# Performance work log

Hardware: AMD Instinct MI355X
Metric: run time of the kernel (lower is better)

Reference implementation:

```python
import jax, jax.numpy as jnp
import numpy as np

OUT = 260        # RESIZE_OUTPUT_IMAGES_SHAPE
TH = 0.8         # OD_SCORE_TH
PCT = 1.0        # INTERNAL_PERCENTAGE_IMAGE_TOTAKE
N_BOXES = 10     # loop bound in original call()
TAPS = 6         # lanczos3 support (radius 3 -> 6 taps, antialias=False)


def _lanczos_taps(src, size):
    """src: (OUT,) float sample coords in crop-local space; size: traced int crop size.
    Returns clamped tap indices (OUT,6) and normalized lanczos3 weights (OUT,6)."""
    base = jnp.floor(src).astype(jnp.int32) - 2
    taps = base[:, None] + jnp.arange(TAPS, dtype=jnp.int32)          # (OUT,6)
    d = src[:, None] - taps.astype(src.dtype)
    w = jnp.where(jnp.abs(d) < 3.0, jnp.sinc(d) * jnp.sinc(d / 3.0), 0.0)
    w = w / jnp.sum(w, axis=1, keepdims=True)
    idx = jnp.clip(taps, 0, size - 1)
    return idx, w


def _crop_resize(img, box):
    """img: (H,W,3). box: (4,) normalized [ymin,xmin,ymax,xmax] -> (OUT,OUT,3).
    Matches tf.image.resize lanczos3 (antialias=False): half-pixel centers, clamped edges."""
    H, W = img.shape[0], img.shape[1]
    y0 = (box[0] * H).astype(jnp.int32)
    x0 = (box[1] * W).astype(jnp.int32)
    y1 = (box[2] * H).astype(jnp.int32)
    x1 = (box[3] * W).astype(jnp.int32)
    ch = jnp.maximum(y1 - y0, 1)
    cw = jnp.maximum(x1 - x0, 1)
    o = jnp.arange(OUT, dtype=img.dtype)
    src_h = (o + 0.5) * (ch.astype(img.dtype) / OUT) - 0.5
    src_w = (o + 0.5) * (cw.astype(img.dtype) / OUT) - 0.5
    idx_h, w_h = _lanczos_taps(src_h, ch)
    idx_w, w_w = _lanczos_taps(src_w, cw)
    idx_h = idx_h + y0
    idx_w = idx_w + x0
    # vertical pass: gather 6 row taps per output row, reduce -> (OUT, W, 3)
    rows = jnp.einsum('pa,pawc->pwc', w_h, img[idx_h])
    # horizontal pass: gather 6 col taps per output col, reduce -> (OUT, OUT, 3)
    out = jnp.einsum('qb,pqbc->pqc', w_w, rows[:, idx_w])
    return out


def setup_inputs() -> dict:
    key = jax.random.key(0)
    k1, k2, k3, k4 = jax.random.split(key, 4)
    # scores: first 10 mostly above threshold, rest below
    s_hi = 0.85 + 0.15 * jax.random.uniform(k1, (N_BOXES,), dtype=jnp.float32)
    s_lo = 0.8 * jax.random.uniform(k2, (100 - N_BOXES,), dtype=jnp.float32)
    od_scores = jnp.concatenate([s_hi, s_lo])
    # bboxes (ymin,xmin,ymax,xmax) with guaranteed positive crop sizes
    u = jax.random.uniform(k3, (100, 4), dtype=jnp.float32)
    od_bboxes = jnp.stack([u[:, 0] * 0.45, u[:, 1] * 0.45,
                           0.55 + 0.45 * u[:, 2], 0.55 + 0.45 * u[:, 3]], axis=1)
    image = jax.random.normal(k4, (1, 2048, 2048, 3), dtype=jnp.float32)
    return {"od_scores": od_scores, "od_bboxes": od_bboxes, "image": image}


def reference(od_scores, od_bboxes, image):
    img = image[0]                           # (H,W,3)
    b10 = od_bboxes[:N_BOXES]
    s10 = od_scores[:N_BOXES]
    valid = ((od_scores[0] >= TH) & (s10 >= TH)
             & (b10[:, 1] >= 0.5 - PCT / 2.0)
             & (b10[:, 3] <= 0.5 + PCT / 2.0))
    crops = jax.vmap(lambda b: _crop_resize(img, b))(b10)   # (10,OUT,OUT,3)
    return crops * valid[:, None, None, None].astype(img.dtype)
```

## Files before the change

### kernel.cpp

```cpp
#include <hip/hip_runtime.h>
#include <math.h>

#define OUT 260
#define TAPS 6
#define IMG_H 2048
#define IMG_W 2048
#define ROW_F (IMG_W * 3)
#define NB 10
#define TH 0.8f
#define QB 65
#define SEGS 4
#define LDSF 1600

__device__ __forceinline__ float sincf(float x) {
    if (x == 0.0f) return 1.0f;
    float px = 3.14159265358979323846f * x;
    return __sinf(px) / px;
}


__global__ __launch_bounds__(320) void tables_kernel(
    const float* __restrict__ scores, const float* __restrict__ boxes,
    float* __restrict__ htab, float* __restrict__ vtab)
{
    const int box = blockIdx.x;
    const float b0 = boxes[box * 4 + 0];
    const float b1 = boxes[box * 4 + 1];
    const float b2 = boxes[box * 4 + 2];
    const float b3 = boxes[box * 4 + 3];

    const int y0 = (int)(b0 * (float)IMG_H);
    const int x0 = (int)(b1 * (float)IMG_W);
    const int y1 = (int)(b2 * (float)IMG_H);
    const int x1 = (int)(b3 * (float)IMG_W);
    const int ch = max(y1 - y0, 1);
    const int cw = max(x1 - x0, 1);

    const bool valid = (scores[0] >= TH) && (scores[box] >= TH)
                    && (b1 >= 0.0f) && (b3 <= 1.0f);
    const float vmask = valid ? 1.0f : 0.0f;

    const int t = threadIdx.x;
    if (t >= OUT) return;

    {
        const float src = ((float)t + 0.5f) * ((float)cw / (float)OUT) - 0.5f;
        const int base = (int)floorf(src) - 2;
        float w[TAPS]; int id[TAPS];
        float s = 0.0f;
        #pragma unroll
        for (int k = 0; k < TAPS; ++k) {
            const float d = src - (float)(base + k);
            const float wv = (fabsf(d) < 3.0f) ? sincf(d) * sincf(d * (1.0f / 3.0f)) : 0.0f;
            w[k] = wv; s += wv;
            int tt = base + k; tt = tt < 0 ? 0 : tt; tt = tt > cw - 1 ? cw - 1 : tt;
            id[k] = (x0 + tt) * 3;
        }
        const float inv = 1.0f / s;
        float* h = htab + ((size_t)(box * OUT + t) << 4);
        int*   hi = (int*)h;
        #pragma unroll
        for (int k = 0; k < TAPS; ++k) { h[k] = w[k] * inv; hi[8 + k] = id[k]; }
        h[6] = 0.0f; h[7] = 0.0f; hi[14] = 0; hi[15] = 0;
    }

    {
        const float src = ((float)t + 0.5f) * ((float)ch / (float)OUT) - 0.5f;
        const int base = (int)floorf(src) - 2;
        float w[TAPS]; int id[TAPS];
        float s = 0.0f;
        #pragma unroll
        for (int k = 0; k < TAPS; ++k) {
            const float d = src - (float)(base + k);
            const float wv = (fabsf(d) < 3.0f) ? sincf(d) * sincf(d * (1.0f / 3.0f)) : 0.0f;
            w[k] = wv; s += wv;
            int tt = base + k; tt = tt < 0 ? 0 : tt; tt = tt > ch - 1 ? ch - 1 : tt;
            id[k] = tt + y0;
        }
        const float inv = vmask / s;
        float* v = vtab + ((size_t)(box * OUT + t) << 4);
        int*   vi = (int*)v;
        #pragma unroll
        for (int k = 0; k < TAPS; ++k) { v[k] = w[k] * inv; vi[8 + k] = id[k]; }
        v[6] = 0.0f; v[7] = 0.0f; vi[14] = 0; vi[15] = 0;
    }
}

__global__ __launch_bounds__(64) void crop_resize_seg(
    const float* __restrict__ img,
    const float* __restrict__ htab,
    const float* __restrict__ vtab,
    float* __restrict__ out)
{
    const int seg = blockIdx.x;
    const int p   = blockIdx.y;
    const int box = blockIdx.z;
    const int q0  = seg * QB;

    const float* vrec = vtab + ((size_t)(box * OUT + p) << 4);
    const int*   vi   = (const int*)vrec;
    float wh[TAPS]; int rows[TAPS];
    #pragma unroll
    for (int k = 0; k < TAPS; ++k) { wh[k] = vrec[k]; rows[k] = vi[8 + k]; }

    const int* hi_first = (const int*)(htab + ((size_t)(box * OUT + q0) << 4));
    const int* hi_last  = (const int*)(htab + ((size_t)(box * OUT + q0 + QB - 1) << 4));
    const int start_f = hi_first[8] & ~3;
    const int n_f     = ((hi_last[13] + 3) - start_f + 3) & ~3;

    __shared__ float lds[LDSF];

    {
        const float* r0 = img + (size_t)rows[0] * ROW_F + start_f;
        const float* r1 = img + (size_t)rows[1] * ROW_F + start_f;
        const float* r2 = img + (size_t)rows[2] * ROW_F + start_f;
        const float* r3 = img + (size_t)rows[3] * ROW_F + start_f;
        const float* r4 = img + (size_t)rows[4] * ROW_F + start_f;
        const float* r5 = img + (size_t)rows[5] * ROW_F + start_f;

        for (int f = threadIdx.x * 4; f < n_f; f += 64 * 4) {
            const float4 v0 = *(const float4*)(r0 + f);
            const float4 v1 = *(const float4*)(r1 + f);
            const float4 v2 = *(const float4*)(r2 + f);
            const float4 v3 = *(const float4*)(r3 + f);
            const float4 v4 = *(const float4*)(r4 + f);
            const float4 v5 = *(const float4*)(r5 + f);
            float4 acc;
            acc.x = wh[0]*v0.x + wh[1]*v1.x + wh[2]*v2.x + wh[3]*v3.x + wh[4]*v4.x + wh[5]*v5.x;
            acc.y = wh[0]*v0.y + wh[1]*v1.y + wh[2]*v2.y + wh[3]*v3.y + wh[4]*v4.y + wh[5]*v5.y;
            acc.z = wh[0]*v0.z + wh[1]*v1.z + wh[2]*v2.z + wh[3]*v3.z + wh[4]*v4.z + wh[5]*v5.z;
            acc.w = wh[0]*v0.w + wh[1]*v1.w + wh[2]*v2.w + wh[3]*v3.w + wh[4]*v4.w + wh[5]*v5.w;
            *(float4*)(lds + f) = acc;
        }
    }
    __syncthreads();

    for (int qi = threadIdx.x; qi < QB; qi += 64) {
        const int q = q0 + qi;
        const float* h  = htab + ((size_t)(box * OUT + q) << 4);
        const int*   hi = (const int*)h;
        float a0 = 0.0f, a1 = 0.0f, a2 = 0.0f;
        #pragma unroll
        for (int k = 0; k < TAPS; ++k) {
            const float w  = h[k];
            const int   li = hi[8 + k] - start_f;
            a0 = fmaf(w, lds[li + 0], a0);
            a1 = fmaf(w, lds[li + 1], a1);
            a2 = fmaf(w, lds[li + 2], a2);
        }
        const size_t o = (((size_t)box * OUT + p) * OUT + q) * 3;
        out[o + 0] = a0;
        out[o + 1] = a1;
        out[o + 2] = a2;
    }
}

__global__ __launch_bounds__(256) void crop_resize_fallback(
    const float* __restrict__ scores, const float* __restrict__ boxes,
    const float* __restrict__ img, float* __restrict__ out)
{
    const int p = blockIdx.x, box = blockIdx.y;
    const float b0 = boxes[box*4+0], b1 = boxes[box*4+1];
    const float b2 = boxes[box*4+2], b3 = boxes[box*4+3];
    const int y0 = (int)(b0*(float)IMG_H), x0 = (int)(b1*(float)IMG_W);
    const int y1 = (int)(b2*(float)IMG_H), x1 = (int)(b3*(float)IMG_W);
    const int ch = max(y1-y0,1), cw = max(x1-x0,1);
    const bool valid = (scores[0]>=TH)&&(scores[box]>=TH)&&(b1>=0.0f)&&(b3<=1.0f);
    const float vmask = valid?1.0f:0.0f;
    float wh[TAPS]; int ih[TAPS];
    {
        const float src = ((float)p+0.5f)*((float)ch/(float)OUT)-0.5f;
        const int base = (int)floorf(src)-2;
        float s = 0.0f;
        #pragma unroll
        for (int a = 0; a < TAPS; ++a) {
            const float d = src-(float)(base+a);
            const float w = (fabsf(d)<3.0f)?sincf(d)*sincf(d*(1.0f/3.0f)):0.0f;
            wh[a]=w; s+=w;
            int t=base+a; t=t<0?0:t; t=t>ch-1?ch-1:t; ih[a]=t+y0;
        }
        const float inv = 1.0f/s;
        #pragma unroll
        for (int a = 0; a < TAPS; ++a) wh[a]*=inv;
    }
    const int start_f = (x0*3)&~3;
    const int end_f = (x0+cw)*3;
    const int n_f = end_f-start_f;
    __shared__ float lds[6152];
    {
        const float* r0 = img+(size_t)ih[0]*ROW_F+start_f;
        const float* r1 = img+(size_t)ih[1]*ROW_F+start_f;
        const float* r2 = img+(size_t)ih[2]*ROW_F+start_f;
        const float* r3 = img+(size_t)ih[3]*ROW_F+start_f;
        const float* r4 = img+(size_t)ih[4]*ROW_F+start_f;
        const float* r5 = img+(size_t)ih[5]*ROW_F+start_f;
        for (int f = threadIdx.x*4; f < n_f; f += 256*4) {
            const float4 v0=*(const float4*)(r0+f), v1=*(const float4*)(r1+f);
            const float4 v2=*(const float4*)(r2+f), v3=*(const float4*)(r3+f);
            const float4 v4=*(const float4*)(r4+f), v5=*(const float4*)(r5+f);
            float4 acc;
            acc.x=wh[0]*v0.x+wh[1]*v1.x+wh[2]*v2.x+wh[3]*v3.x+wh[4]*v4.x+wh[5]*v5.x;
            acc.y=wh[0]*v0.y+wh[1]*v1.y+wh[2]*v2.y+wh[3]*v3.y+wh[4]*v4.y+wh[5]*v5.y;
            acc.z=wh[0]*v0.z+wh[1]*v1.z+wh[2]*v2.z+wh[3]*v3.z+wh[4]*v4.z+wh[5]*v5.z;
            acc.w=wh[0]*v0.w+wh[1]*v1.w+wh[2]*v2.w+wh[3]*v3.w+wh[4]*v4.w+wh[5]*v5.w;
            *(float4*)(lds+f)=acc;
        }
    }
    __syncthreads();
    const float wscale = (float)cw/(float)OUT;
    for (int q = threadIdx.x; q < OUT; q += 256) {
        const float src = ((float)q+0.5f)*wscale-0.5f;
        const int basew = (int)floorf(src)-2;
        float ww[TAPS]; float s = 0.0f;
        #pragma unroll
        for (int k = 0; k < TAPS; ++k) {
            const float d = src-(float)(basew+k);
            const float w = (fabsf(d)<3.0f)?sincf(d)*sincf(d*(1.0f/3.0f)):0.0f;
            ww[k]=w; s+=w;
        }
        const float inv = 1.0f/s;
        float a0=0,a1=0,a2=0;
        #pragma unroll
        for (int k = 0; k < TAPS; ++k) {
            int t=basew+k; t=t<0?0:t; t=t>cw-1?cw-1:t;
            const int hb=(x0+t)*3-start_f;
            a0=fmaf(ww[k],lds[hb+0],a0);
            a1=fmaf(ww[k],lds[hb+1],a1);
            a2=fmaf(ww[k],lds[hb+2],a2);
        }
        const float m = vmask*inv;
        const size_t o = (((size_t)box*OUT+p)*OUT+q)*3;
        out[o+0]=a0*m; out[o+1]=a1*m; out[o+2]=a2*m;
    }
}

extern "C" void kernel_launch(void* const* d_in, const int* in_sizes, int n_in,
                              void* d_out, int out_size, void* d_ws, size_t ws_size,
                              hipStream_t stream) {
    const float* scores = (const float*)d_in[0];
    const float* boxes  = (const float*)d_in[1];
    const float* img    = (const float*)d_in[2];
    float* out = (float*)d_out;

    const size_t tab_bytes = (size_t)NB * OUT * 16 * sizeof(float);
    if (ws_size < 2 * tab_bytes) {
        crop_resize_fallback<<<dim3(OUT, NB), dim3(256), 0, stream>>>(scores, boxes, img, out);
        return;
    }
    float* htab = (float*)d_ws;
    float* vtab = (float*)((char*)d_ws + tab_bytes);

    tables_kernel<<<dim3(NB), dim3(320), 0, stream>>>(scores, boxes, htab, vtab);
    crop_resize_seg<<<dim3(SEGS, OUT, NB), dim3(64), 0, stream>>>(img, htab, vtab, out);
}
```

Before: 113.8 us.

## Fuse table precompute into single crop-resize kernel with XCD-aware block remap

```diff
diff --git a/kernel.cpp b/kernel.cpp
--- a/kernel.cpp
+++ b/kernel.cpp
@@ -8,9 +8,10 @@
 #define ROW_F (IMG_W * 3)
 #define NB 10
 #define TH 0.8f
-#define QB 65
-#define SEGS 4
-#define LDSF 1600
+#define LDSF 6152
+#define NXCD 8
+#define NWG (NB * OUT)
+#define CPX (NWG / NXCD)
 
 __device__ __forceinline__ float sincf(float x) {
     if (x == 0.0f) return 1.0f;
@@ -18,107 +19,77 @@
     return __sinf(px) / px;
 }
 
+__global__ __launch_bounds__(256) void crop_resize_one(
+    const float* __restrict__ scores, const float* __restrict__ boxes,
+    const float* __restrict__ img, float* __restrict__ out)
+{
+    const int bid  = blockIdx.x;
+    const int lbid = (bid & (NXCD - 1)) * CPX + (bid >> 3);
+    const int p    = lbid % OUT;
+    const int box  = lbid / OUT;
 
-__global__ __launch_bounds__(320) void tables_kernel(
-    const float* __restrict__ scores, const float* __restrict__ boxes,
-    float* __restrict__ htab, float* __restrict__ vtab)
-{
-    const int box = blockIdx.x;
     const float b0 = boxes[box * 4 + 0];
     const float b1 = boxes[box * 4 + 1];
     const float b2 = boxes[box * 4 + 2];
     const float b3 = boxes[box * 4 + 3];
-
     const int y0 = (int)(b0 * (float)IMG_H);
     const int x0 = (int)(b1 * (float)IMG_W);
     const int y1 = (int)(b2 * (float)IMG_H);
     const int x1 = (int)(b3 * (float)IMG_W);
     const int ch = max(y1 - y0, 1);
     const int cw = max(x1 - x0, 1);
-
     const bool valid = (scores[0] >= TH) && (scores[box] >= TH)
                     && (b1 >= 0.0f) && (b3 <= 1.0f);
     const float vmask = valid ? 1.0f : 0.0f;
 
-    const int t = threadIdx.x;
-    if (t >= OUT) return;
-
+    float wh[TAPS]; int ih[TAPS];
     {
-        const float src = ((float)t + 0.5f) * ((float)cw / (float)OUT) - 0.5f;
+        const float src = ((float)p + 0.5f) * ((float)ch / (float)OUT) - 0.5f;
         const int base = (int)floorf(src) - 2;
-        float w[TAPS]; int id[TAPS];
         float s = 0.0f;
         #pragma unroll
         for (int k = 0; k < TAPS; ++k) {
             const float d = src - (float)(base + k);
-            const float wv = (fabsf(d) < 3.0f) ? sincf(d) * sincf(d * (1.0f / 3.0f)) : 0.0f;
-            w[k] = wv; s += wv;
-            int tt = base + k; tt = tt < 0 ? 0 : tt; tt = tt > cw - 1 ? cw - 1 : tt;
-            id[k] = (x0 + tt) * 3;
+            const float w = (fabsf(d) < 3.0f) ? sincf(d) * sincf(d * (1.0f / 3.0f)) : 0.0f;
+            wh[k] = w; s += w;
+            int t = base + k; t = t < 0 ? 0 : t; t = t > ch - 1 ? ch - 1 : t;
+            ih[k] = t + y0;
         }
         const float inv = 1.0f / s;
-        float* h = htab + ((size_t)(box * OUT + t) << 4);
-        int*   hi = (int*)h;
         #pragma unroll
-        for (int k = 0; k < TAPS; ++k) { h[k] = w[k] * inv; hi[8 + k] = id[k]; }
-        h[6] = 0.0f; h[7] = 0.0f; hi[14] = 0; hi[15] = 0;
+        for (int k = 0; k < TAPS; ++k) wh[k] *= inv;
     }
 
+    const int start_f = (x0 * 3) & ~3;
+    const int n_f     = (x0 + cw) * 3 - start_f;
+
+    const int q = threadIdx.x;
+    const float wscale = (float)cw / (float)OUT;
+    float ww[TAPS]; int lb[TAPS]; float hm;
     {
-        const float src = ((float)t + 0.5f) * ((float)ch / (float)OUT) - 0.5f;
+        const float src = ((float)q + 0.5f) * wscale - 0.5f;
         const int base = (int)floorf(src) - 2;
-        float w[TAPS]; int id[TAPS];
         float s = 0.0f;
         #pragma unroll
         for (int k = 0; k < TAPS; ++k) {
             const float d = src - (float)(base + k);
-            const float wv = (fabsf(d) < 3.0f) ? sincf(d) * sincf(d * (1.0f / 3.0f)) : 0.0f;
-            w[k] = wv; s += wv;
-            int tt = base + k; tt = tt < 0 ? 0 : tt; tt = tt > ch - 1 ? ch - 1 : tt;
-            id[k] = tt + y0;
+            const float w = (fabsf(d) < 3.0f) ? sincf(d) * sincf(d * (1.0f / 3.0f)) : 0.0f;
+            ww[k] = w; s += w;
+            int t = base + k; t = t < 0 ? 0 : t; t = t > cw - 1 ? cw - 1 : t;
+            lb[k] = (x0 + t) * 3 - start_f;
         }
-        const float inv = vmask / s;
-        float* v = vtab + ((size_t)(box * OUT + t) << 4);
-        int*   vi = (int*)v;
-        #pragma unroll
-        for (int k = 0; k < TAPS; ++k) { v[k] = w[k] * inv; vi[8 + k] = id[k]; }
-        v[6] = 0.0f; v[7] = 0.0f; vi[14] = 0; vi[15] = 0;
+        hm = vmask / s;
     }
-}
-
-__global__ __launch_bounds__(64) void crop_resize_seg(
-    const float* __restrict__ img,
-    const float* __restrict__ htab,
-    const float* __restrict__ vtab,
-    float* __restrict__ out)
-{
-    const int seg = blockIdx.x;
-    const int p   = blockIdx.y;
-    const int box = blockIdx.z;
-    const int q0  = seg * QB;
-
-    const float* vrec = vtab + ((size_t)(box * OUT + p) << 4);
-    const int*   vi   = (const int*)vrec;
-    float wh[TAPS]; int rows[TAPS];
-    #pragma unroll
-    for (int k = 0; k < TAPS; ++k) { wh[k] = vrec[k]; rows[k] = vi[8 + k]; }
-
-    const int* hi_first = (const int*)(htab + ((size_t)(box * OUT + q0) << 4));
-    const int* hi_last  = (const int*)(htab + ((size_t)(box * OUT + q0 + QB - 1) << 4));
-    const int start_f = hi_first[8] & ~3;
-    const int n_f     = ((hi_last[13] + 3) - start_f + 3) & ~3;
 
     __shared__ float lds[LDSF];
-
     {
-        const float* r0 = img + (size_t)rows[0] * ROW_F + start_f;
-        const float* r1 = img + (size_t)rows[1] * ROW_F + start_f;
-        const float* r2 = img + (size_t)rows[2] * ROW_F + start_f;
-        const float* r3 = img + (size_t)rows[3] * ROW_F + start_f;
-        const float* r4 = img + (size_t)rows[4] * ROW_F + start_f;
-        const float* r5 = img + (size_t)rows[5] * ROW_F + start_f;
-
-        for (int f = threadIdx.x * 4; f < n_f; f += 64 * 4) {
+        const float* r0 = img + (size_t)ih[0] * ROW_F + start_f;
+        const float* r1 = img + (size_t)ih[1] * ROW_F + start_f;
+        const float* r2 = img + (size_t)ih[2] * ROW_F + start_f;
+        const float* r3 = img + (size_t)ih[3] * ROW_F + start_f;
+        const float* r4 = img + (size_t)ih[4] * ROW_F + start_f;
+        const float* r5 = img + (size_t)ih[5] * ROW_F + start_f;
+        for (int f = threadIdx.x * 4; f < n_f; f += 256 * 4) {
             const float4 v0 = *(const float4*)(r0 + f);
             const float4 v1 = *(const float4*)(r1 + f);
             const float4 v2 = *(const float4*)(r2 + f);
@@ -135,102 +106,45 @@
     }
     __syncthreads();
 
-    for (int qi = threadIdx.x; qi < QB; qi += 64) {
-        const int q = q0 + qi;
-        const float* h  = htab + ((size_t)(box * OUT + q) << 4);
-        const int*   hi = (const int*)h;
+    {
         float a0 = 0.0f, a1 = 0.0f, a2 = 0.0f;
         #pragma unroll
         for (int k = 0; k < TAPS; ++k) {
-            const float w  = h[k];
-            const int   li = hi[8 + k] - start_f;
-            a0 = fmaf(w, lds[li + 0], a0);
-            a1 = fmaf(w, lds[li + 1], a1);
-            a2 = fmaf(w, lds[li + 2], a2);
+            a0 = fmaf(ww[k], lds[lb[k] + 0], a0);
+            a1 = fmaf(ww[k], lds[lb[k] + 1], a1);
+            a2 = fmaf(ww[k], lds[lb[k] + 2], a2);
         }
         const size_t o = (((size_t)box * OUT + p) * OUT + q) * 3;
-        out[o + 0] = a0;
-        out[o + 1] = a1;
-        out[o + 2] = a2;
+        out[o + 0] = a0 * hm;
+        out[o + 1] = a1 * hm;
+        out[o + 2] = a2 * hm;
     }
-}
 
-__global__ __launch_bounds__(256) void crop_resize_fallback(
-    const float* __restrict__ scores, const float* __restrict__ boxes,
-    const float* __restrict__ img, float* __restrict__ out)
-{
-    const int p = blockIdx.x, box = blockIdx.y;
-    const float b0 = boxes[box*4+0], b1 = boxes[box*4+1];
-    const float b2 = boxes[box*4+2], b3 = boxes[box*4+3];
-    const int y0 = (int)(b0*(float)IMG_H), x0 = (int)(b1*(float)IMG_W);
-    const int y1 = (int)(b2*(float)IMG_H), x1 = (int)(b3*(float)IMG_W);
-    const int ch = max(y1-y0,1), cw = max(x1-x0,1);
-    const bool valid = (scores[0]>=TH)&&(scores[box]>=TH)&&(b1>=0.0f)&&(b3<=1.0f);
-    const float vmask = valid?1.0f:0.0f;
-    float wh[TAPS]; int ih[TAPS];
-    {
-        const float src = ((float)p+0.5f)*((float)ch/(float)OUT)-0.5f;
-        const int base = (int)floorf(src)-2;
-        float s = 0.0f;
-        #pragma unroll
-        for (int a = 0; a < TAPS; ++a) {
-            const float d = src-(float)(base+a);
-            const float w = (fabsf(d)<3.0f)?sincf(d)*sincf(d*(1.0f/3.0f)):0.0f;
-            wh[a]=w; s+=w;
-            int t=base+a; t=t<0?0:t; t=t>ch-1?ch-1:t; ih[a]=t+y0;
-        }
-        const float inv = 1.0f/s;
-        #pragma unroll
-        for (int a = 0; a < TAPS; ++a) wh[a]*=inv;
-    }
-    const int start_f = (x0*3)&~3;
-    const int end_f = (x0+cw)*3;
-    const int n_f = end_f-start_f;
-    __shared__ float lds[6152];
-    {
-        const float* r0 = img+(size_t)ih[0]*ROW_F+start_f;
-        const float* r1 = img+(size_t)ih[1]*ROW_F+start_f;
-        const float* r2 = img+(size_t)ih[2]*ROW_F+start_f;
-        const float* r3 = img+(size_t)ih[3]*ROW_F+start_f;
-        const float* r4 = img+(size_t)ih[4]*ROW_F+start_f;
-        const float* r5 = img+(size_t)ih[5]*ROW_F+start_f;
-        for (int f = threadIdx.x*4; f < n_f; f += 256*4) {
-            const float4 v0=*(const float4*)(r0+f), v1=*(const float4*)(r1+f);
-            const float4 v2=*(const float4*)(r2+f), v3=*(const float4*)(r3+f);
-            const float4 v4=*(const float4*)(r4+f), v5=*(const float4*)(r5+f);
-            float4 acc;
-            acc.x=wh[0]*v0.x+wh[1]*v1.x+wh[2]*v2.x+wh[3]*v3.x+wh[4]*v4.x+wh[5]*v5.x;
-            acc.y=wh[0]*v0.y+wh[1]*v1.y+wh[2]*v2.y+wh[3]*v3.y+wh[4]*v4.y+wh[5]*v5.y;
-            acc.z=wh[0]*v0.z+wh[1]*v1.z+wh[2]*v2.z+wh[3]*v3.z+wh[4]*v4.z+wh[5]*v5.z;
-            acc.w=wh[0]*v0.w+wh[1]*v1.w+wh[2]*v2.w+wh[3]*v3.w+wh[4]*v4.w+wh[5]*v5.w;
-            *(float4*)(lds+f)=acc;
-        }
-    }
-    __syncthreads();
-    const float wscale = (float)cw/(float)OUT;
-    for (int q = threadIdx.x; q < OUT; q += 256) {
-        const float src = ((float)q+0.5f)*wscale-0.5f;
-        const int basew = (int)floorf(src)-2;
-        float ww[TAPS]; float s = 0.0f;
+    if (threadIdx.x < OUT - 256) {
+        const int q2 = 256 + threadIdx.x;
+        const float src = ((float)q2 + 0.5f) * wscale - 0.5f;
+        const int base = (int)floorf(src) - 2;
+        float w2[TAPS]; int l2i[TAPS]; float s = 0.0f;
         #pragma unroll
         for (int k = 0; k < TAPS; ++k) {
-            const float d = src-(float)(basew+k);
-            const float w = (fabsf(d)<3.0f)?sincf(d)*sincf(d*(1.0f/3.0f)):0.0f;
-            ww[k]=w; s+=w;
+            const float d = src - (float)(base + k);
+            const float w = (fabsf(d) < 3.0f) ? sincf(d) * sincf(d * (1.0f / 3.0f)) : 0.0f;
+            w2[k] = w; s += w;
+            int t = base + k; t = t < 0 ? 0 : t; t = t > cw - 1 ? cw - 1 : t;
+            l2i[k] = (x0 + t) * 3 - start_f;
         }
-        const float inv = 1.0f/s;
-        float a0=0,a1=0,a2=0;
+        const float m2 = vmask / s;
+        float a0 = 0.0f, a1 = 0.0f, a2 = 0.0f;
         #pragma unroll
         for (int k = 0; k < TAPS; ++k) {
-            int t=basew+k; t=t<0?0:t; t=t>cw-1?cw-1:t;
-            const int hb=(x0+t)*3-start_f;
-            a0=fmaf(ww[k],lds[hb+0],a0);
-            a1=fmaf(ww[k],lds[hb+1],a1);
-            a2=fmaf(ww[k],lds[hb+2],a2);
+            a0 = fmaf(w2[k], lds[l2i[k] + 0], a0);
+            a1 = fmaf(w2[k], lds[l2i[k] + 1], a1);
+            a2 = fmaf(w2[k], lds[l2i[k] + 2], a2);
         }
-        const float m = vmask*inv;
-        const size_t o = (((size_t)box*OUT+p)*OUT+q)*3;
-        out[o+0]=a0*m; out[o+1]=a1*m; out[o+2]=a2*m;
+        const size_t o = (((size_t)box * OUT + p) * OUT + q2) * 3;
+        out[o + 0] = a0 * m2;
+        out[o + 1] = a1 * m2;
+        out[o + 2] = a2 * m2;
     }
 }
 
@@ -241,15 +155,5 @@
     const float* boxes  = (const float*)d_in[1];
     const float* img    = (const float*)d_in[2];
     float* out = (float*)d_out;
-
-    const size_t tab_bytes = (size_t)NB * OUT * 16 * sizeof(float);
-    if (ws_size < 2 * tab_bytes) {
-        crop_resize_fallback<<<dim3(OUT, NB), dim3(256), 0, stream>>>(scores, boxes, img, out);
-        return;
-    }
-    float* htab = (float*)d_ws;
-    float* vtab = (float*)((char*)d_ws + tab_bytes);
-
-    tables_kernel<<<dim3(NB), dim3(320), 0, stream>>>(scores, boxes, htab, vtab);
-    crop_resize_seg<<<dim3(SEGS, OUT, NB), dim3(64), 0, stream>>>(img, htab, vtab, out);
+    crop_resize_one<<<dim3(NWG), dim3(256), 0, stream>>>(scores, boxes, img, out);
 }
```

New measurement: 112.5 us. No clear change (-1.1%).
